# Kernel tuning notes

Hardware: AMD Instinct MI355X
Metric: run time of the kernel (lower is better)

The kernel has to match this reference:

```python
import jax, jax.numpy as jnp
import numpy as np

N_NODES = 100000
N_EDGES = 400000   # number of hyperedges
N_INC = 1600000    # incidence pairs (node, hyperedge)
N_GRAPHS = 512
ATOM_DIM = 92
NODE_DIM = 64
H_DIM = 128
NUM_LAYERS = 3
BN_EPS = 1e-5


def setup_inputs() -> dict:
    key = jax.random.key(0)
    ks = jax.random.split(key, 10)
    x = jax.random.normal(ks[0], (N_NODES, ATOM_DIM), jnp.float32)
    node_idx = jax.random.randint(ks[1], (N_INC,), 0, N_NODES)
    edge_idx = jax.random.randint(ks[2], (N_INC,), 0, N_EDGES)
    batch = jnp.sort(jax.random.randint(ks[3], (N_NODES,), 0, N_GRAPHS))

    def lin(k, fan_in, shape):
        return jax.random.normal(k, shape, jnp.float32) / np.float32(np.sqrt(fan_in))

    W_emb = lin(ks[4], ATOM_DIM, (ATOM_DIM, NODE_DIM))
    b_emb = jnp.zeros((NODE_DIM,), jnp.float32)
    conv_W = lin(ks[5], NODE_DIM, (NUM_LAYERS, NODE_DIM, NODE_DIM))
    conv_b = jnp.zeros((NUM_LAYERS, NODE_DIM), jnp.float32)
    bn_gamma = jnp.ones((NUM_LAYERS, NODE_DIM), jnp.float32)
    bn_beta = jnp.zeros((NUM_LAYERS, NODE_DIM), jnp.float32)
    fc_W = lin(ks[6], NODE_DIM, (NODE_DIM, H_DIM))
    fc_b = jnp.zeros((H_DIM,), jnp.float32)
    fco_W = lin(ks[7], H_DIM, (H_DIM, 1))
    fco_b = jnp.zeros((1,), jnp.float32)
    return {
        "x": x, "W_emb": W_emb, "b_emb": b_emb,
        "conv_W": conv_W, "conv_b": conv_b,
        "bn_gamma": bn_gamma, "bn_beta": bn_beta,
        "fc_W": fc_W, "fc_b": fc_b, "fco_W": fco_W, "fco_b": fco_b,
        "node_idx": node_idx, "edge_idx": edge_idx, "batch": batch,
    }


def _hypergraph_conv(h, W, b, gamma, beta, node_idx, edge_idx):
    """PyG-style HypergraphConv: X' = D^-1 H B^-1 H^T (X Theta), then BN + softplus."""
    h = h @ W + b  # [N, F]
    ones = jnp.ones((N_INC,), h.dtype)
    deg_e = jax.ops.segment_sum(ones, edge_idx, num_segments=N_EDGES)  # |e| per hyperedge
    Binv = jnp.where(deg_e > 0, 1.0 / deg_e, 0.0)
    # node -> hyperedge: mean of member node features
    e_feat = jax.ops.segment_sum(h[node_idx], edge_idx, num_segments=N_EDGES) * Binv[:, None]
    deg_n = jax.ops.segment_sum(ones, node_idx, num_segments=N_NODES)  # node hyperedge-degree
    Dinv = jnp.where(deg_n > 0, 1.0 / deg_n, 0.0)
    # hyperedge -> node
    out = jax.ops.segment_sum(e_feat[edge_idx], node_idx, num_segments=N_NODES) * Dinv[:, None]
    # BatchNorm1d over node dimension (training-mode batch statistics, biased var)
    mean = out.mean(axis=0)
    var = jnp.mean(jnp.square(out - mean), axis=0)
    out = gamma * (out - mean) * jax.lax.rsqrt(var + BN_EPS) + beta
    return jax.nn.softplus(out)


def reference(x, W_emb, b_emb, conv_W, conv_b, bn_gamma, bn_beta,
              fc_W, fc_b, fco_W, fco_b, node_idx, edge_idx, batch):
    h = x @ W_emb + b_emb  # [N, node_dim]
    for l in range(NUM_LAYERS):
        h = _hypergraph_conv(h, conv_W[l], conv_b[l], bn_gamma[l], bn_beta[l],
                             node_idx, edge_idx)
    # scatter-mean pooling over graphs
    cnt = jax.ops.segment_sum(jnp.ones((N_NODES,), h.dtype), batch, num_segments=N_GRAPHS)
    pooled = jax.ops.segment_sum(h, batch, num_segments=N_GRAPHS) / jnp.maximum(cnt, 1.0)[:, None]
    g = jax.nn.softplus(pooled)
    g = jax.nn.softplus(g @ fc_W + fc_b)
    return g @ fco_W + fco_b  # [N_GRAPHS, 1]
```

## Files before the change

### kernel.cpp

```cpp
#include <hip/hip_runtime.h>
#include <hip/hip_fp16.h>
#include <math.h>

#define N_NODES   100000
#define N_EDGES   400000
#define N_INC     1600000
#define N_GRAPHS  512
#define ATOM_DIM  92
#define NODE_DIM  64
#define H_DIM     128
#define NUM_LAYERS 3
#define BN_EPS    1e-5f

#define NBUCK     391
#define PCHUNK    2048
#define NCHP      ((N_INC + PCHUNK - 1) / PCHUNK)
#define MM_BLOCKS 1568

struct alignas(8)  half4 { __half2 a, b; };
struct alignas(16) half8 { __half2 a, b, c, d; };
typedef __attribute__((ext_vector_type(8))) float float8;
typedef __attribute__((ext_vector_type(2))) float float2v;
typedef __attribute__((ext_vector_type(4))) float f32x4;
typedef _Float16 f16x8 __attribute__((ext_vector_type(8)));

__device__ __forceinline__ float softplus_f(float x) {
    return fmaxf(x, 0.f) + log1pf(expf(-fabsf(x)));
}

__device__ __forceinline__ float8 cvt8(half8 v) {
    float2 p0 = __half22float2(v.a), p1 = __half22float2(v.b);
    float2 p2 = __half22float2(v.c), p3 = __half22float2(v.d);
    float8 r;
    r[0] = p0.x; r[1] = p0.y; r[2] = p1.x; r[3] = p1.y;
    r[4] = p2.x; r[5] = p2.y; r[6] = p3.x; r[7] = p3.y;
    return r;
}
__device__ __forceinline__ half8 cvt16(float8 v) {
    half8 r;
    r.a = __floats2half2_rn(v[0], v[1]);
    r.b = __floats2half2_rn(v[2], v[3]);
    r.c = __floats2half2_rn(v[4], v[5]);
    r.d = __floats2half2_rn(v[6], v[7]);
    return r;
}

__device__ __forceinline__ float8 fp8x8_to_f32(uint2 v) {
    float2v l0 = __builtin_amdgcn_cvt_pk_f32_fp8((int)v.x, false);
    float2v h0 = __builtin_amdgcn_cvt_pk_f32_fp8((int)v.x, true);
    float2v l1 = __builtin_amdgcn_cvt_pk_f32_fp8((int)v.y, false);
    float2v h1 = __builtin_amdgcn_cvt_pk_f32_fp8((int)v.y, true);
    float8 r;
    r[0] = l0.x; r[1] = l0.y; r[2] = h0.x; r[3] = h0.y;
    r[4] = l1.x; r[5] = l1.y; r[6] = h1.x; r[7] = h1.y;
    return r;
}
__device__ __forceinline__ uint2 f32_to_fp8x8(float8 v) {
    int a = 0, b = 0;
    a = __builtin_amdgcn_cvt_pk_fp8_f32(v[0], v[1], a, false);
    a = __builtin_amdgcn_cvt_pk_fp8_f32(v[2], v[3], a, true);
    b = __builtin_amdgcn_cvt_pk_fp8_f32(v[4], v[5], b, false);
    b = __builtin_amdgcn_cvt_pk_fp8_f32(v[6], v[7], b, true);
    uint2 r; r.x = (unsigned)a; r.y = (unsigned)b;
    return r;
}


__global__ void __launch_bounds__(256) embed_mfma(
        const float* __restrict__ x, const float* __restrict__ W,
        const float* __restrict__ bvec, uint2* __restrict__ h8) {
    __shared__ half8 so8[4][16][9];
    int tid = threadIdx.x;
    int w = tid >> 6, lane = tid & 63;
    int l15 = lane & 15, rg = lane >> 4;
    __half* so_h = (__half*)so8[w];

    f16x8 bf[4][3];
    #pragma unroll
    for (int c = 0; c < 4; ++c)
        #pragma unroll
        for (int kk = 0; kk < 3; ++kk)
            #pragma unroll
            for (int j = 0; j < 8; ++j) {
                int k = kk * 32 + rg * 8 + j;
                bf[c][kk][j] = (k < ATOM_DIM) ? (_Float16)W[k * 64 + c * 16 + l15]
                                              : (_Float16)0.f;
            }
    float bias[4];
    #pragma unroll
    for (int c = 0; c < 4; ++c) bias[c] = bvec[c * 16 + l15];

    int wave_global = blockIdx.x * 4 + w;
    for (int tile = wave_global; tile < N_NODES / 16; tile += MM_BLOCKS * 4) {
        int n0 = tile * 16;
        const float* xrow = x + (size_t)(n0 + l15) * ATOM_DIM;
        f16x8 af[3];
        #pragma unroll
        for (int kk = 0; kk < 3; ++kk) {
            int k0 = kk * 32 + rg * 8;
            if (k0 + 8 <= ATOM_DIM) {
                float4 v0 = *(const float4*)&xrow[k0];
                float4 v1 = *(const float4*)&xrow[k0 + 4];
                af[kk][0] = (_Float16)v0.x; af[kk][1] = (_Float16)v0.y;
                af[kk][2] = (_Float16)v0.z; af[kk][3] = (_Float16)v0.w;
                af[kk][4] = (_Float16)v1.x; af[kk][5] = (_Float16)v1.y;
                af[kk][6] = (_Float16)v1.z; af[kk][7] = (_Float16)v1.w;
            } else {
                float4 v0 = *(const float4*)&xrow[88];
                af[kk][0] = (_Float16)v0.x; af[kk][1] = (_Float16)v0.y;
                af[kk][2] = (_Float16)v0.z; af[kk][3] = (_Float16)v0.w;
                af[kk][4] = (_Float16)0.f;  af[kk][5] = (_Float16)0.f;
                af[kk][6] = (_Float16)0.f;  af[kk][7] = (_Float16)0.f;
            }
        }
        #pragma unroll
        for (int c = 0; c < 4; ++c) {
            f32x4 acc = {0.f, 0.f, 0.f, 0.f};
            acc = __builtin_amdgcn_mfma_f32_16x16x32_f16(af[0], bf[c][0], acc, 0, 0, 0);
            acc = __builtin_amdgcn_mfma_f32_16x16x32_f16(af[1], bf[c][1], acc, 0, 0, 0);
            acc = __builtin_amdgcn_mfma_f32_16x16x32_f16(af[2], bf[c][2], acc, 0, 0, 0);
            #pragma unroll
            for (int i = 0; i < 4; ++i)
                so_h[(rg * 4 + i) * 72 + c * 16 + l15] = __float2half_rn(acc[i] + bias[c]);
        }
        #pragma unroll
        for (int it = 0; it < 2; ++it) {
            int row = (lane >> 3) + it * 8;
            half8 v = *(half8*)&so_h[row * 72 + (lane & 7) * 8];
            h8[(size_t)(n0 + row) * 8 + (lane & 7)] = f32_to_fp8x8(cvt8(v));
        }
    }
}


__global__ void __launch_bounds__(256) part_hist(
        const int* __restrict__ key, int n, int shift, int* __restrict__ hists) {
    __shared__ int h[NBUCK];
    int tid = threadIdx.x;
    int base = blockIdx.x * PCHUNK;
    for (int i = tid; i < NBUCK; i += 256) h[i] = 0;
    __syncthreads();
    #pragma unroll
    for (int k = 0; k < 8; ++k) {
        int i = base + tid + k * 256;
        if (i < n) atomicAdd(&h[key[i] >> shift], 1);
    }
    __syncthreads();
    for (int i = tid; i < NBUCK; i += 256)
        hists[(size_t)blockIdx.x * NBUCK + i] = h[i];
}

__global__ void __launch_bounds__(256) col_scan(
        int* __restrict__ hists, int nch, int* __restrict__ colsum) {
    __shared__ int ws[256];
    int i = blockIdx.x, tid = threadIdx.x;
    int v[4];
    int loc = 0;
    #pragma unroll
    for (int k = 0; k < 4; ++k) {
        int b = tid * 4 + k;
        v[k] = (b < nch) ? hists[(size_t)b * NBUCK + i] : 0;
        loc += v[k];
    }
    ws[tid] = loc;
    __syncthreads();
    for (int off = 1; off < 256; off <<= 1) {
        int t = (tid >= off) ? ws[tid - off] : 0;
        __syncthreads();
        ws[tid] += t;
        __syncthreads();
    }
    int run = ws[tid] - loc;
    if (tid == 255) colsum[i] = ws[255];
    #pragma unroll
    for (int k = 0; k < 4; ++k) {
        int b = tid * 4 + k;
        if (b < nch) hists[(size_t)b * NBUCK + i] = run;
        run += v[k];
    }
}

__global__ void bbase_scan(const int* __restrict__ colsum, int* __restrict__ bbase) {
    __shared__ int sh[512];
    int tid = threadIdx.x;
    int v = (tid < NBUCK) ? colsum[tid] : 0;
    sh[tid] = v;
    __syncthreads();
    for (int off = 1; off < 512; off <<= 1) {
        int t = (tid >= off) ? sh[tid - off] : 0;
        __syncthreads();
        sh[tid] += t;
        __syncthreads();
    }
    if (tid <= NBUCK)
        bbase[tid] = (tid == 0) ? 0 : sh[tid - 1];
}

__global__ void __launch_bounds__(256) part_scatter(
        const int* __restrict__ key, const int* __restrict__ pay,
        int n, int shift, const int* __restrict__ hists, const int* __restrict__ bbase,
        unsigned long long* __restrict__ staging) {
    __shared__ int cur[NBUCK];
    int tid = threadIdx.x;
    int base = blockIdx.x * PCHUNK;
    int keys[8], pays[8];
    #pragma unroll
    for (int k = 0; k < 8; ++k) {
        int i = base + tid + k * 256;
        bool ok = (i < n);
        keys[k] = ok ? key[i] : -1;
        pays[k] = ok ? pay[i] : 0;
    }
    for (int i = tid; i < NBUCK; i += 256)
        cur[i] = bbase[i] + hists[(size_t)blockIdx.x * NBUCK + i];
    __syncthreads();
    #pragma unroll
    for (int k = 0; k < 8; ++k) {
        if (keys[k] >= 0) {
            int pos = atomicAdd(&cur[keys[k] >> shift], 1);
            staging[pos] = ((unsigned long long)(unsigned)keys[k] << 32) | (unsigned)pays[k];
        }
    }
}

template<int RANGE>
__global__ void bucket_finalize(const unsigned long long* __restrict__ staging,
                                const int* __restrict__ bbase,
                                int nIds, float* __restrict__ inv,
                                int* __restrict__ off, int* __restrict__ list) {
    __shared__ int hist[RANGE];
    __shared__ int wsum[256];
    const int PER = RANGE / 256;
    int b = blockIdx.x, tid = threadIdx.x;
    int s = bbase[b], t = bbase[b + 1];
    int id0 = b * RANGE;
    for (int i = tid; i < RANGE; i += 256) hist[i] = 0;
    __syncthreads();
    for (int j = s + tid; j < t; j += 256) {
        int key = (int)(staging[j] >> 32);
        atomicAdd(&hist[key - id0], 1);
    }
    __syncthreads();
    int base0 = tid * PER;
    int vals[PER];
    int local = 0;
    #pragma unroll
    for (int k = 0; k < PER; ++k) { vals[k] = hist[base0 + k]; local += vals[k]; }
    wsum[tid] = local;
    __syncthreads();
    for (int o = 1; o < 256; o <<= 1) {
        int tv = (tid >= o) ? wsum[tid - o] : 0;
        __syncthreads();
        wsum[tid] += tv;
        __syncthreads();
    }
    int run = wsum[tid] - local;
    #pragma unroll
    for (int k = 0; k < PER; ++k) {
        int id = id0 + base0 + k;
        int gpos = s + run;
        if (id < nIds) {
            off[id] = gpos;
            inv[id] = vals[k] > 0 ? 1.f / (float)vals[k] : 0.f;
        } else if (id == nIds) {
            off[nIds] = gpos;
        }
        hist[base0 + k] = gpos;
        run += vals[k];
    }
    __syncthreads();
    for (int j = s + tid; j < t; j += 256) {
        unsigned long long it = staging[j];
        int key = (int)(it >> 32);
        int pos = atomicAdd(&hist[key - id0], 1);
        list[pos] = (int)(it & 0xffffffffu);
    }
}


__global__ void __launch_bounds__(256) edge_agg(
        const int* __restrict__ eoff, const int* __restrict__ elist,
        const uint2* __restrict__ h8, const float* __restrict__ binv,
        uint2* __restrict__ efeat8) {
    int e = blockIdx.x * 32 + (threadIdx.x >> 3);
    int q = threadIdx.x & 7;
    int s = eoff[e], t = eoff[e + 1];
    float8 acc0 = (float8)0.f, acc1 = (float8)0.f;
    int j = s;
    for (; j + 1 < t; j += 2) {
        int n0 = __ldg(&elist[j]), n1 = __ldg(&elist[j + 1]);
        acc0 += fp8x8_to_f32(__ldg(&h8[(size_t)n0 * 8 + q]));
        acc1 += fp8x8_to_f32(__ldg(&h8[(size_t)n1 * 8 + q]));
    }
    if (j < t)
        acc0 += fp8x8_to_f32(__ldg(&h8[(size_t)__ldg(&elist[j]) * 8 + q]));
    acc0 += acc1;
    acc0 *= binv[e];
    efeat8[(size_t)e * 8 + q] = f32_to_fp8x8(acc0);
}

__global__ void __launch_bounds__(256) node_agg(
        const int* __restrict__ noff, const int* __restrict__ nlist,
        const uint2* __restrict__ efeat8, const float* __restrict__ dinv,
        __half* __restrict__ agg16) {
    int n = blockIdx.x * 32 + (threadIdx.x >> 3);
    int q = threadIdx.x & 7;
    int s = noff[n], t = noff[n + 1];
    float8 acc0 = (float8)0.f, acc1 = (float8)0.f;
    int j = s;
    for (; j + 1 < t; j += 2) {
        int e0 = __ldg(&nlist[j]), e1 = __ldg(&nlist[j + 1]);
        acc0 += fp8x8_to_f32(__ldg(&efeat8[(size_t)e0 * 8 + q]));
        acc1 += fp8x8_to_f32(__ldg(&efeat8[(size_t)e1 * 8 + q]));
    }
    if (j < t)
        acc0 += fp8x8_to_f32(__ldg(&efeat8[(size_t)__ldg(&nlist[j]) * 8 + q]));
    acc0 += acc1;
    acc0 *= dinv[n];
    half8 r = cvt16(acc0);
    *(half8*)&agg16[(size_t)n * 64 + q * 8] = r;
}


__global__ void __launch_bounds__(256) gemm_bn_kernel(
        const __half* __restrict__ agg16, const float* __restrict__ dinv,
        const float* __restrict__ W, const float* __restrict__ bvec,
        __half* __restrict__ outr16, float* __restrict__ partials) {
    __shared__ half8 so8[4][16][9];
    __shared__ float sred[4][128];
    int tid = threadIdx.x;
    int w = tid >> 6, lane = tid & 63;
    int l15 = lane & 15, rg = lane >> 4;
    __half* so_h = (__half*)so8[w];

    f16x8 bf[4][2];
    #pragma unroll
    for (int c = 0; c < 4; ++c)
        #pragma unroll
        for (int kk = 0; kk < 2; ++kk)
            #pragma unroll
            for (int j = 0; j < 8; ++j) {
                int k = kk * 32 + rg * 8 + j;
                bf[c][kk][j] = (_Float16)W[k * 64 + c * 16 + l15];
            }
    float bias[4];
    #pragma unroll
    for (int c = 0; c < 4; ++c) bias[c] = bvec[c * 16 + l15];

    float sa[4] = {0.f, 0.f, 0.f, 0.f}, sb[4] = {0.f, 0.f, 0.f, 0.f};
    int wave_global = blockIdx.x * 4 + w;
    for (int tile = wave_global; tile < N_NODES / 16; tile += MM_BLOCKS * 4) {
        int n0 = tile * 16;
        f16x8 a0 = *(const f16x8*)&agg16[(size_t)(n0 + l15) * 64 + rg * 8];
        f16x8 a1 = *(const f16x8*)&agg16[(size_t)(n0 + l15) * 64 + 32 + rg * 8];
        float dv[4];
        #pragma unroll
        for (int i = 0; i < 4; ++i) dv[i] = dinv[n0 + rg * 4 + i];
        #pragma unroll
        for (int c = 0; c < 4; ++c) {
            f32x4 acc = {0.f, 0.f, 0.f, 0.f};
            acc = __builtin_amdgcn_mfma_f32_16x16x32_f16(a0, bf[c][0], acc, 0, 0, 0);
            acc = __builtin_amdgcn_mfma_f32_16x16x32_f16(a1, bf[c][1], acc, 0, 0, 0);
            #pragma unroll
            for (int i = 0; i < 4; ++i) {
                float vv = (dv[i] > 0.f) ? (acc[i] + bias[c]) : 0.f;
                sa[c] += vv; sb[c] += vv * vv;
                so_h[(rg * 4 + i) * 72 + c * 16 + l15] = __float2half_rn(vv);
            }
        }
        #pragma unroll
        for (int it = 0; it < 2; ++it) {
            int row = (lane >> 3) + it * 8;
            half8 v = *(half8*)&so_h[row * 72 + (lane & 7) * 8];
            *(half8*)&outr16[(size_t)(n0 + row) * 64 + (lane & 7) * 8] = v;
        }
    }
    #pragma unroll
    for (int c = 0; c < 4; ++c) {
        sa[c] += __shfl_xor(sa[c], 16); sa[c] += __shfl_xor(sa[c], 32);
        sb[c] += __shfl_xor(sb[c], 16); sb[c] += __shfl_xor(sb[c], 32);
    }
    if (rg == 0) {
        #pragma unroll
        for (int c = 0; c < 4; ++c) {
            sred[w][c * 16 + l15]      = sa[c];
            sred[w][64 + c * 16 + l15] = sb[c];
        }
    }
    __syncthreads();
    if (tid < 128) {
        float v = sred[0][tid] + sred[1][tid] + sred[2][tid] + sred[3][tid];
        partials[(size_t)blockIdx.x * 128 + tid] = v;
    }
}


__global__ void __launch_bounds__(256) reduce_bnfin(
        const float* __restrict__ partials, const float* __restrict__ gamma,
        const float* __restrict__ beta, float* __restrict__ scsh) {
    __shared__ float ra[256];
    __shared__ float rb[256];
    int f = blockIdx.x, tid = threadIdx.x;
    float a = 0.f, b = 0.f;
    for (int j = tid; j < MM_BLOCKS; j += 256) {
        a += partials[(size_t)j * 128 + f];
        b += partials[(size_t)j * 128 + 64 + f];
    }
    ra[tid] = a; rb[tid] = b;
    __syncthreads();
    for (int s = 128; s > 0; s >>= 1) {
        if (tid < s) { ra[tid] += ra[tid + s]; rb[tid] += rb[tid + s]; }
        __syncthreads();
    }
    if (tid == 0) {
        const float invN = 1.f / (float)N_NODES;
        float mean = ra[0] * invN;
        float var  = rb[0] * invN - mean * mean;
        var = fmaxf(var, 0.f);
        float sc = gamma[f] * rsqrtf(var + BN_EPS);
        scsh[f]      = sc;
        scsh[64 + f] = beta[f] - mean * sc;
    }
}


__global__ void apply_kernel(const half8* __restrict__ outr8, const float* __restrict__ scsh,
                             uint2* __restrict__ h8) {
    int gid = blockIdx.x * 256 + threadIdx.x;
    if (gid >= N_NODES * 8) return;
    int qq = gid & 7;
    float8 v = cvt8(outr8[gid]);
    float4 sc0 = ((const float4*)scsh)[qq * 2];
    float4 sc1 = ((const float4*)scsh)[qq * 2 + 1];
    float4 sh0 = ((const float4*)(scsh + 64))[qq * 2];
    float4 sh1 = ((const float4*)(scsh + 64))[qq * 2 + 1];
    float8 r;
    r[0] = softplus_f(fmaf(v[0], sc0.x, sh0.x));
    r[1] = softplus_f(fmaf(v[1], sc0.y, sh0.y));
    r[2] = softplus_f(fmaf(v[2], sc0.z, sh0.z));
    r[3] = softplus_f(fmaf(v[3], sc0.w, sh0.w));
    r[4] = softplus_f(fmaf(v[4], sc1.x, sh1.x));
    r[5] = softplus_f(fmaf(v[5], sc1.y, sh1.y));
    r[6] = softplus_f(fmaf(v[6], sc1.z, sh1.z));
    r[7] = softplus_f(fmaf(v[7], sc1.w, sh1.w));
    h8[gid] = f32_to_fp8x8(r);
}


__global__ void graph_bounds(const int* __restrict__ batch, int* __restrict__ goff) {
    int g = blockIdx.x * 256 + threadIdx.x;
    if (g > N_GRAPHS) return;
    int lo = 0, hi = N_NODES;
    while (lo < hi) {
        int mid = (lo + hi) >> 1;
        if (batch[mid] < g) lo = mid + 1; else hi = mid;
    }
    goff[g] = lo;
}

__global__ void pool_head_kernel(const uint2* __restrict__ h8, const int* __restrict__ goff,
                                 const float* __restrict__ fcW, const float* __restrict__ fcb,
                                 const float* __restrict__ fcoW, const float* __restrict__ fcob,
                                 float* __restrict__ out) {
    __shared__ float8 part[32][8];
    __shared__ float p[64];
    __shared__ float red[128];
    int g = blockIdx.x, tid = threadIdx.x;
    int s = goff[g], t = goff[g + 1];
    int r = tid >> 3, q = tid & 7;
    float8 acc = (float8)0.f;
    for (int n = s + r; n < t; n += 32)
        acc += fp8x8_to_f32(__ldg(&h8[(size_t)n * 8 + q]));
    part[r][q] = acc;
    __syncthreads();
    for (int st = 16; st >= 1; st >>= 1) {
        if (r < st) part[r][q] += part[r + st][q];
        __syncthreads();
    }
    if (tid < 8) {
        float c = fmaxf((float)(t - s), 1.f);
        float8 v = part[0][tid];
        #pragma unroll
        for (int jj = 0; jj < 8; ++jj)
            p[tid * 8 + jj] = softplus_f(v[jj] / c);
    }
    __syncthreads();
    if (tid < 128) {
        float a = fcb[tid];
        #pragma unroll
        for (int k = 0; k < 64; ++k)
            a = fmaf(p[k], fcW[k * H_DIM + tid], a);
        red[tid] = softplus_f(a) * fcoW[tid];
    }
    __syncthreads();
    for (int st = 64; st > 0; st >>= 1) {
        if (tid < st) red[tid] += red[tid + st];
        __syncthreads();
    }
    if (tid == 0) out[g] = red[0] + fcob[0];
}


extern "C" void kernel_launch(void* const* d_in, const int* in_sizes, int n_in,
                              void* d_out, int out_size, void* d_ws, size_t ws_size,
                              hipStream_t stream) {
    const float* x      = (const float*)d_in[0];
    const float* W_emb  = (const float*)d_in[1];
    const float* b_emb  = (const float*)d_in[2];
    const float* conv_W = (const float*)d_in[3];
    const float* conv_b = (const float*)d_in[4];
    const float* bn_g   = (const float*)d_in[5];
    const float* bn_b   = (const float*)d_in[6];
    const float* fc_W   = (const float*)d_in[7];
    const float* fc_b   = (const float*)d_in[8];
    const float* fco_W  = (const float*)d_in[9];
    const float* fco_b  = (const float*)d_in[10];
    const int* node_idx = (const int*)d_in[11];
    const int* edge_idx = (const int*)d_in[12];
    const int* batch    = (const int*)d_in[13];
    float* out = (float*)d_out;

    uint2*  h8     = (uint2*)d_ws;
    __half* outr16 = (__half*)(h8 + (size_t)N_NODES * 8);
    __half* agg16  = outr16 + (size_t)N_NODES * 64;
    uint2*  efeat8 = (uint2*)(agg16 + (size_t)N_NODES * 64);
    unsigned long long* staging = (unsigned long long*)(efeat8 + (size_t)N_EDGES * 8);
    float* binv    = (float*)(staging + N_INC);
    float* dinv    = binv   + N_EDGES;
    float* scsh    = dinv   + N_NODES;
    float* partials= scsh   + 128;
    int*   goff    = (int*)(partials + (size_t)MM_BLOCKS * 128);
    int*   eoff    = goff  + N_GRAPHS + 1;
    int*   noff    = eoff  + N_EDGES + 1;
    int*   hists   = noff  + N_NODES + 1;
    int*   colsum  = hists + (size_t)NCHP * NBUCK;
    int*   bbaseE  = colsum + NBUCK;
    int*   bbaseN  = bbaseE + NBUCK + 1;
    int*   elist   = bbaseN + NBUCK + 1;
    int*   nlist   = elist + N_INC;

    part_hist<<<NCHP, 256, 0, stream>>>(edge_idx, N_INC, 10, hists);
    col_scan<<<NBUCK, 256, 0, stream>>>(hists, NCHP, colsum);
    bbase_scan<<<1, 512, 0, stream>>>(colsum, bbaseE);
    part_scatter<<<NCHP, 256, 0, stream>>>(edge_idx, node_idx, N_INC, 10, hists, bbaseE, staging);
    bucket_finalize<1024><<<NBUCK, 256, 0, stream>>>(staging, bbaseE, N_EDGES, binv, eoff, elist);
    part_hist<<<NCHP, 256, 0, stream>>>(node_idx, N_INC, 8, hists);
    col_scan<<<NBUCK, 256, 0, stream>>>(hists, NCHP, colsum);
    bbase_scan<<<1, 512, 0, stream>>>(colsum, bbaseN);
    part_scatter<<<NCHP, 256, 0, stream>>>(node_idx, edge_idx, N_INC, 8, hists, bbaseN, staging);
    bucket_finalize<256><<<NBUCK, 256, 0, stream>>>(staging, bbaseN, N_NODES, dinv, noff, nlist);

    graph_bounds<<<(N_GRAPHS + 1 + 255) / 256, 256, 0, stream>>>(batch, goff);

    embed_mfma<<<MM_BLOCKS, 256, 0, stream>>>(x, W_emb, b_emb, h8);

    for (int l = 0; l < NUM_LAYERS; ++l) {
        const float* Wl = conv_W + (size_t)l * NODE_DIM * NODE_DIM;
        const float* bl = conv_b + (size_t)l * NODE_DIM;

        edge_agg<<<N_EDGES / 32, 256, 0, stream>>>(eoff, elist, (const uint2*)h8,
                                                   binv, efeat8);
        node_agg<<<N_NODES / 32, 256, 0, stream>>>(noff, nlist, (const uint2*)efeat8,
                                                   dinv, agg16);
        gemm_bn_kernel<<<MM_BLOCKS, 256, 0, stream>>>(agg16, dinv, Wl, bl, outr16, partials);
        reduce_bnfin<<<64, 256, 0, stream>>>(partials, bn_g + (size_t)l * 64,
                                             bn_b + (size_t)l * 64, scsh);
        apply_kernel<<<(N_NODES * 8 + 255) / 256, 256, 0, stream>>>((const half8*)outr16, scsh, h8);
    }

    pool_head_kernel<<<N_GRAPHS, 256, 0, stream>>>(h8, goff, fc_W, fc_b, fco_W, fco_b, out);
}
```

Before: 435.2 us.

## Fuse dual CSR partitioning passes and widen gather loads to 16 bytes

The two CSR build pipelines (by edge and by node) are merged into dual kernels, so the incidence arrays are read once and launch count drops, using separate staging buffers. The edge and node aggregation kernels now use 4 threads per row with 16-byte loads instead of 8 threads with 8-byte loads, giving more rows per block and fewer memory transactions per gather. In exchange each thread needs more registers, and each block has fewer independent threads per row.

```diff
diff --git a/kernel.cpp b/kernel.cpp
--- a/kernel.cpp
+++ b/kernel.cpp
@@ -45,15 +45,18 @@
     return r;
 }
 
-__device__ __forceinline__ float8 fp8x8_to_f32(uint2 v) {
-    float2v l0 = __builtin_amdgcn_cvt_pk_f32_fp8((int)v.x, false);
-    float2v h0 = __builtin_amdgcn_cvt_pk_f32_fp8((int)v.x, true);
-    float2v l1 = __builtin_amdgcn_cvt_pk_f32_fp8((int)v.y, false);
-    float2v h1 = __builtin_amdgcn_cvt_pk_f32_fp8((int)v.y, true);
+__device__ __forceinline__ float8 fp8x8_to_f32u(unsigned lo, unsigned hi) {
+    float2v l0 = __builtin_amdgcn_cvt_pk_f32_fp8((int)lo, false);
+    float2v h0 = __builtin_amdgcn_cvt_pk_f32_fp8((int)lo, true);
+    float2v l1 = __builtin_amdgcn_cvt_pk_f32_fp8((int)hi, false);
+    float2v h1 = __builtin_amdgcn_cvt_pk_f32_fp8((int)hi, true);
     float8 r;
     r[0] = l0.x; r[1] = l0.y; r[2] = h0.x; r[3] = h0.y;
     r[4] = l1.x; r[5] = l1.y; r[6] = h1.x; r[7] = h1.y;
     return r;
+}
+__device__ __forceinline__ float8 fp8x8_to_f32(uint2 v) {
+    return fp8x8_to_f32u(v.x, v.y);
 }
 __device__ __forceinline__ uint2 f32_to_fp8x8(float8 v) {
     int a = 0, b = 0;
@@ -133,33 +136,45 @@
 }
 
 
-__global__ void __launch_bounds__(256) part_hist(
-        const int* __restrict__ key, int n, int shift, int* __restrict__ hists) {
-    __shared__ int h[NBUCK];
+__global__ void __launch_bounds__(256) part_hist_dual(
+        const int* __restrict__ ekey, const int* __restrict__ nkey,
+        int* __restrict__ histsE, int* __restrict__ histsN) {
+    __shared__ int hE[NBUCK];
+    __shared__ int hN[NBUCK];
     int tid = threadIdx.x;
     int base = blockIdx.x * PCHUNK;
-    for (int i = tid; i < NBUCK; i += 256) h[i] = 0;
+    for (int i = tid; i < NBUCK; i += 256) { hE[i] = 0; hN[i] = 0; }
     __syncthreads();
     #pragma unroll
     for (int k = 0; k < 8; ++k) {
         int i = base + tid + k * 256;
-        if (i < n) atomicAdd(&h[key[i] >> shift], 1);
-    }
-    __syncthreads();
-    for (int i = tid; i < NBUCK; i += 256)
-        hists[(size_t)blockIdx.x * NBUCK + i] = h[i];
-}
-
-__global__ void __launch_bounds__(256) col_scan(
-        int* __restrict__ hists, int nch, int* __restrict__ colsum) {
+        if (i < N_INC) {
+            atomicAdd(&hE[ekey[i] >> 10], 1);
+            atomicAdd(&hN[nkey[i] >> 8], 1);
+        }
+    }
+    __syncthreads();
+    for (int i = tid; i < NBUCK; i += 256) {
+        histsE[(size_t)blockIdx.x * NBUCK + i] = hE[i];
+        histsN[(size_t)blockIdx.x * NBUCK + i] = hN[i];
+    }
+}
+
+__global__ void __launch_bounds__(256) col_scan_dual(
+        int* __restrict__ histsE, int* __restrict__ histsN,
+        int* __restrict__ colsumE, int* __restrict__ colsumN) {
     __shared__ int ws[256];
-    int i = blockIdx.x, tid = threadIdx.x;
+    int which = blockIdx.x >= NBUCK;
+    int i = which ? (blockIdx.x - NBUCK) : blockIdx.x;
+    int* hists = which ? histsN : histsE;
+    int* colsum = which ? colsumN : colsumE;
+    int tid = threadIdx.x;
     int v[4];
     int loc = 0;
     #pragma unroll
     for (int k = 0; k < 4; ++k) {
         int b = tid * 4 + k;
-        v[k] = (b < nch) ? hists[(size_t)b * NBUCK + i] : 0;
+        v[k] = (b < NCHP) ? hists[(size_t)b * NBUCK + i] : 0;
         loc += v[k];
     }
     ws[tid] = loc;
@@ -175,13 +190,16 @@
     #pragma unroll
     for (int k = 0; k < 4; ++k) {
         int b = tid * 4 + k;
-        if (b < nch) hists[(size_t)b * NBUCK + i] = run;
+        if (b < NCHP) hists[(size_t)b * NBUCK + i] = run;
         run += v[k];
     }
 }
 
-__global__ void bbase_scan(const int* __restrict__ colsum, int* __restrict__ bbase) {
+__global__ void bbase_scan_dual(const int* __restrict__ colsumE, const int* __restrict__ colsumN,
+                                int* __restrict__ bbaseE, int* __restrict__ bbaseN) {
     __shared__ int sh[512];
+    const int* colsum = blockIdx.x ? colsumN : colsumE;
+    int* bbase = blockIdx.x ? bbaseN : bbaseE;
     int tid = threadIdx.x;
     int v = (tid < NBUCK) ? colsum[tid] : 0;
     sh[tid] = v;
@@ -196,29 +214,36 @@
         bbase[tid] = (tid == 0) ? 0 : sh[tid - 1];
 }
 
-__global__ void __launch_bounds__(256) part_scatter(
-        const int* __restrict__ key, const int* __restrict__ pay,
-        int n, int shift, const int* __restrict__ hists, const int* __restrict__ bbase,
-        unsigned long long* __restrict__ staging) {
-    __shared__ int cur[NBUCK];
+__global__ void __launch_bounds__(256) part_scatter_dual(
+        const int* __restrict__ ekey, const int* __restrict__ nkey,
+        const int* __restrict__ histsE, const int* __restrict__ histsN,
+        const int* __restrict__ bbaseE, const int* __restrict__ bbaseN,
+        unsigned long long* __restrict__ stagingE,
+        unsigned long long* __restrict__ stagingN) {
+    __shared__ int curE[NBUCK];
+    __shared__ int curN[NBUCK];
     int tid = threadIdx.x;
     int base = blockIdx.x * PCHUNK;
-    int keys[8], pays[8];
+    int kE[8], kN[8];
     #pragma unroll
     for (int k = 0; k < 8; ++k) {
         int i = base + tid + k * 256;
-        bool ok = (i < n);
-        keys[k] = ok ? key[i] : -1;
-        pays[k] = ok ? pay[i] : 0;
-    }
-    for (int i = tid; i < NBUCK; i += 256)
-        cur[i] = bbase[i] + hists[(size_t)blockIdx.x * NBUCK + i];
+        bool ok = (i < N_INC);
+        kE[k] = ok ? ekey[i] : -1;
+        kN[k] = ok ? nkey[i] : 0;
+    }
+    for (int i = tid; i < NBUCK; i += 256) {
+        curE[i] = bbaseE[i] + histsE[(size_t)blockIdx.x * NBUCK + i];
+        curN[i] = bbaseN[i] + histsN[(size_t)blockIdx.x * NBUCK + i];
+    }
     __syncthreads();
     #pragma unroll
     for (int k = 0; k < 8; ++k) {
-        if (keys[k] >= 0) {
-            int pos = atomicAdd(&cur[keys[k] >> shift], 1);
-            staging[pos] = ((unsigned long long)(unsigned)keys[k] << 32) | (unsigned)pays[k];
+        if (kE[k] >= 0) {
+            int pe = atomicAdd(&curE[kE[k] >> 10], 1);
+            stagingE[pe] = ((unsigned long long)(unsigned)kE[k] << 32) | (unsigned)kN[k];
+            int pn = atomicAdd(&curN[kN[k] >> 8], 1);
+            stagingN[pn] = ((unsigned long long)(unsigned)kN[k] << 32) | (unsigned)kE[k];
         }
     }
 }
@@ -280,45 +305,61 @@
 
 __global__ void __launch_bounds__(256) edge_agg(
         const int* __restrict__ eoff, const int* __restrict__ elist,
-        const uint2* __restrict__ h8, const float* __restrict__ binv,
-        uint2* __restrict__ efeat8) {
-    int e = blockIdx.x * 32 + (threadIdx.x >> 3);
-    int q = threadIdx.x & 7;
+        const uint4* __restrict__ h16B, const float* __restrict__ binv,
+        uint4* __restrict__ efeat16B) {
+    int e = blockIdx.x * 64 + (threadIdx.x >> 2);
+    if (e >= N_EDGES) return;
+    int q = threadIdx.x & 3;
     int s = eoff[e], t = eoff[e + 1];
-    float8 acc0 = (float8)0.f, acc1 = (float8)0.f;
+    float8 alo = (float8)0.f, ahi = (float8)0.f;
+    float8 blo = (float8)0.f, bhi = (float8)0.f;
     int j = s;
     for (; j + 1 < t; j += 2) {
         int n0 = __ldg(&elist[j]), n1 = __ldg(&elist[j + 1]);
-        acc0 += fp8x8_to_f32(__ldg(&h8[(size_t)n0 * 8 + q]));
-        acc1 += fp8x8_to_f32(__ldg(&h8[(size_t)n1 * 8 + q]));
-    }
-    if (j < t)
-        acc0 += fp8x8_to_f32(__ldg(&h8[(size_t)__ldg(&elist[j]) * 8 + q]));
-    acc0 += acc1;
-    acc0 *= binv[e];
-    efeat8[(size_t)e * 8 + q] = f32_to_fp8x8(acc0);
+        uint4 v0 = __ldg(&h16B[(size_t)n0 * 4 + q]);
+        uint4 v1 = __ldg(&h16B[(size_t)n1 * 4 + q]);
+        alo += fp8x8_to_f32u(v0.x, v0.y); ahi += fp8x8_to_f32u(v0.z, v0.w);
+        blo += fp8x8_to_f32u(v1.x, v1.y); bhi += fp8x8_to_f32u(v1.z, v1.w);
+    }
+    if (j < t) {
+        uint4 v0 = __ldg(&h16B[(size_t)__ldg(&elist[j]) * 4 + q]);
+        alo += fp8x8_to_f32u(v0.x, v0.y); ahi += fp8x8_to_f32u(v0.z, v0.w);
+    }
+    alo += blo; ahi += bhi;
+    float bv = binv[e];
+    alo *= bv; ahi *= bv;
+    uint2 lo = f32_to_fp8x8(alo), hi = f32_to_fp8x8(ahi);
+    uint4 st; st.x = lo.x; st.y = lo.y; st.z = hi.x; st.w = hi.y;
+    efeat16B[(size_t)e * 4 + q] = st;
 }
 
 __global__ void __launch_bounds__(256) node_agg(
         const int* __restrict__ noff, const int* __restrict__ nlist,
-        const uint2* __restrict__ efeat8, const float* __restrict__ dinv,
+        const uint4* __restrict__ efeat16B, const float* __restrict__ dinv,
         __half* __restrict__ agg16) {
-    int n = blockIdx.x * 32 + (threadIdx.x >> 3);
-    int q = threadIdx.x & 7;
+    int n = blockIdx.x * 64 + (threadIdx.x >> 2);
+    if (n >= N_NODES) return;
+    int q = threadIdx.x & 3;
     int s = noff[n], t = noff[n + 1];
-    float8 acc0 = (float8)0.f, acc1 = (float8)0.f;
+    float8 alo = (float8)0.f, ahi = (float8)0.f;
+    float8 blo = (float8)0.f, bhi = (float8)0.f;
     int j = s;
     for (; j + 1 < t; j += 2) {
         int e0 = __ldg(&nlist[j]), e1 = __ldg(&nlist[j + 1]);
-        acc0 += fp8x8_to_f32(__ldg(&efeat8[(size_t)e0 * 8 + q]));
-        acc1 += fp8x8_to_f32(__ldg(&efeat8[(size_t)e1 * 8 + q]));
-    }
-    if (j < t)
-        acc0 += fp8x8_to_f32(__ldg(&efeat8[(size_t)__ldg(&nlist[j]) * 8 + q]));
-    acc0 += acc1;
-    acc0 *= dinv[n];
-    half8 r = cvt16(acc0);
-    *(half8*)&agg16[(size_t)n * 64 + q * 8] = r;
+        uint4 v0 = __ldg(&efeat16B[(size_t)e0 * 4 + q]);
+        uint4 v1 = __ldg(&efeat16B[(size_t)e1 * 4 + q]);
+        alo += fp8x8_to_f32u(v0.x, v0.y); ahi += fp8x8_to_f32u(v0.z, v0.w);
+        blo += fp8x8_to_f32u(v1.x, v1.y); bhi += fp8x8_to_f32u(v1.z, v1.w);
+    }
+    if (j < t) {
+        uint4 v0 = __ldg(&efeat16B[(size_t)__ldg(&nlist[j]) * 4 + q]);
+        alo += fp8x8_to_f32u(v0.x, v0.y); ahi += fp8x8_to_f32u(v0.z, v0.w);
+    }
+    alo += blo; ahi += bhi;
+    float dv = dinv[n];
+    alo *= dv; ahi *= dv;
+    *(half8*)&agg16[(size_t)n * 64 + q * 16]     = cvt16(alo);
+    *(half8*)&agg16[(size_t)n * 64 + q * 16 + 8] = cvt16(ahi);
 }
 
 
@@ -520,35 +561,35 @@
     const int* batch    = (const int*)d_in[13];
     float* out = (float*)d_out;
 
-    uint2*  h8     = (uint2*)d_ws;
-    __half* outr16 = (__half*)(h8 + (size_t)N_NODES * 8);
-    __half* agg16  = outr16 + (size_t)N_NODES * 64;
-    uint2*  efeat8 = (uint2*)(agg16 + (size_t)N_NODES * 64);
-    unsigned long long* staging = (unsigned long long*)(efeat8 + (size_t)N_EDGES * 8);
-    float* binv    = (float*)(staging + N_INC);
+    uint2*  h8      = (uint2*)d_ws;
+    __half* outr16  = (__half*)(h8 + (size_t)N_NODES * 8);
+    __half* agg16   = outr16 + (size_t)N_NODES * 64;
+    uint2*  efeat8  = (uint2*)(agg16 + (size_t)N_NODES * 64);
+    unsigned long long* stagingE = (unsigned long long*)(efeat8 + (size_t)N_EDGES * 8);
+    unsigned long long* stagingN = stagingE + N_INC;
+    float* binv    = (float*)(stagingN + N_INC);
     float* dinv    = binv   + N_EDGES;
     float* scsh    = dinv   + N_NODES;
     float* partials= scsh   + 128;
     int*   goff    = (int*)(partials + (size_t)MM_BLOCKS * 128);
     int*   eoff    = goff  + N_GRAPHS + 1;
     int*   noff    = eoff  + N_EDGES + 1;
-    int*   hists   = noff  + N_NODES + 1;
-    int*   colsum  = hists + (size_t)NCHP * NBUCK;
-    int*   bbaseE  = colsum + NBUCK;
+    int*   histsE  = noff  + N_NODES + 1;
+    int*   histsN  = histsE + (size_t)NCHP * NBUCK;
+    int*   colsumE = histsN + (size_t)NCHP * NBUCK;
+    int*   colsumN = colsumE + NBUCK;
+    int*   bbaseE  = colsumN + NBUCK;
     int*   bbaseN  = bbaseE + NBUCK + 1;
     int*   elist   = bbaseN + NBUCK + 1;
     int*   nlist   = elist + N_INC;
 
-    part_hist<<<NCHP, 256, 0, stream>>>(edge_idx, N_INC, 10, hists);
-    col_scan<<<NBUCK, 256, 0, stream>>>(hists, NCHP, colsum);
-    bbase_scan<<<1, 512, 0, stream>>>(colsum, bbaseE);
-    part_scatter<<<NCHP, 256, 0, stream>>>(edge_idx, node_idx, N_INC, 10, hists, bbaseE, staging);
-    bucket_finalize<1024><<<NBUCK, 256, 0, stream>>>(staging, bbaseE, N_EDGES, binv, eoff, elist);
-    part_hist<<<NCHP, 256, 0, stream>>>(node_idx, N_INC, 8, hists);
-    col_scan<<<NBUCK, 256, 0, stream>>>(hists, NCHP, colsum);
-    bbase_scan<<<1, 512, 0, stream>>>(colsum, bbaseN);
-    part_scatter<<<NCHP, 256, 0, stream>>>(node_idx, edge_idx, N_INC, 8, hists, bbaseN, staging);
-    bucket_finalize<256><<<NBUCK, 256, 0, stream>>>(staging, bbaseN, N_NODES, dinv, noff, nlist);
+    part_hist_dual<<<NCHP, 256, 0, stream>>>(edge_idx, node_idx, histsE, histsN);
+    col_scan_dual<<<2 * NBUCK, 256, 0, stream>>>(histsE, histsN, colsumE, colsumN);
+    bbase_scan_dual<<<2, 512, 0, stream>>>(colsumE, colsumN, bbaseE, bbaseN);
+    part_scatter_dual<<<NCHP, 256, 0, stream>>>(edge_idx, node_idx, histsE, histsN,
+                                                bbaseE, bbaseN, stagingE, stagingN);
+    bucket_finalize<1024><<<NBUCK, 256, 0, stream>>>(stagingE, bbaseE, N_EDGES, binv, eoff, elist);
+    bucket_finalize<256><<<NBUCK, 256, 0, stream>>>(stagingN, bbaseN, N_NODES, dinv, noff, nlist);
 
     graph_bounds<<<(N_GRAPHS + 1 + 255) / 256, 256, 0, stream>>>(batch, goff);
 
@@ -558,10 +599,10 @@
         const float* Wl = conv_W + (size_t)l * NODE_DIM * NODE_DIM;
         const float* bl = conv_b + (size_t)l * NODE_DIM;
 
-        edge_agg<<<N_EDGES / 32, 256, 0, stream>>>(eoff, elist, (const uint2*)h8,
-                                                   binv, efeat8);
-        node_agg<<<N_NODES / 32, 256, 0, stream>>>(noff, nlist, (const uint2*)efeat8,
-                                                   dinv, agg16);
+        edge_agg<<<(N_EDGES + 63) / 64, 256, 0, stream>>>(eoff, elist, (const uint4*)h8,
+                                                          binv, (uint4*)efeat8);
+        node_agg<<<(N_NODES + 63) / 64, 256, 0, stream>>>(noff, nlist, (const uint4*)efeat8,
+                                                          dinv, agg16);
         gemm_bn_kernel<<<MM_BLOCKS, 256, 0, stream>>>(agg16, dinv, Wl, bl, outr16, partials);
         reduce_bnfin<<<64, 256, 0, stream>>>(partials, bn_g + (size_t)l * 64,
                                              bn_b + (size_t)l * 64, scsh);
```

Measured after the change: 408.8 us. 6.1% less time.
